# Optimization experiments

Measured on AMD Instinct MI355X. Metric: run time of the kernel, lower is better.

Reference implementation:

```python
import jax, jax.numpy as jnp
import numpy as np

B, T, D, MP = 32, 256, 512, 20


def setup_inputs() -> dict:
    key = jax.random.key(0)
    k1, k2, k3 = jax.random.split(key, 3)
    reps_lt = jax.random.normal(k1, (B, T, D), dtype=jnp.float32)
    reps_rt = jax.random.normal(k2, (B, T, D), dtype=jnp.float32)
    kernel = jax.random.normal(k3, (1, 1, 1, MP, D), dtype=jnp.float32)
    return {"reps_lt": reps_lt, "reps_rt": reps_rt, "kernel": kernel}


def reference(reps_lt, reps_rt, kernel):
    # kernel: (1,1,1,m,d) -> (m,d)
    km = kernel.reshape(kernel.shape[-2], kernel.shape[-1])
    # scores[b,t,s,m] = sum_d lt[b,t,d] * km[m,d] * rt[b,s,d]
    # matches original broadcast-multiply + sum over d (cosine_norm=False path)
    scores = jnp.einsum('btd,md,bsd->btsm', reps_lt, km, reps_rt)
    match = jnp.tanh(scores)               # [b, t1, t2, m]
    return jnp.max(match, axis=2)          # max-pool over t2 -> [b, t1, m]
```

## Files before the change

kernel.cpp:

```cpp
#include <hip/hip_runtime.h>


constexpr int TT = 256;
constexpr int DD = 512;
constexpr int NM = 20;
constexpr int NB = 32;
constexpr int BM = 64;

typedef float f32x4 __attribute__((ext_vector_type(4)));
typedef int   i32x8 __attribute__((ext_vector_type(8)));

__device__ __forceinline__ unsigned pack_bf16(float lo, float hi) {
    unsigned ulo = __builtin_bit_cast(unsigned, lo);
    unsigned uhi = __builtin_bit_cast(unsigned, hi);
    return (ulo >> 16) | (uhi & 0xFFFF0000u);
}

__device__ __forceinline__ unsigned pk4_fp8(float a, float b, float c, float d) {
    unsigned r = __builtin_amdgcn_cvt_pk_fp8_f32(a, b, 0, false);
    return __builtin_amdgcn_cvt_pk_fp8_f32(c, d, r, true);
}

__global__ __launch_bounds__(256)
void cast_rt(const float* __restrict__ rt, unsigned char* __restrict__ rtf)
{
    const int bid = (int)blockIdx.x;
    const int c8  = bid & 7;
    const int i   = bid >> 3;
    const int b   = c8 + 8 * (i & 3);
    const int sub = i >> 2;
    const int tid = threadIdx.x;
    const int lane = tid & 63;
    const int u6  = sub * 4 + (tid >> 6);
    const int s   = (u6 & 15) * 16 + (lane & 15);
    const int d0  = (u6 >> 4) * 128 + (lane >> 4) * 32;

    const float* p = rt + ((size_t)b * TT + s) * DD + d0;
    float4 x0 = *(const float4*)p;
    float4 x1 = *(const float4*)(p + 4);
    float4 x2 = *(const float4*)(p + 8);
    float4 x3 = *(const float4*)(p + 12);
    float4 x4 = *(const float4*)(p + 16);
    float4 x5 = *(const float4*)(p + 20);
    float4 x6 = *(const float4*)(p + 24);
    float4 x7 = *(const float4*)(p + 28);
    uint4 w0, w1;
    w0.x = pk4_fp8(x0.x, x0.y, x0.z, x0.w);
    w0.y = pk4_fp8(x1.x, x1.y, x1.z, x1.w);
    w0.z = pk4_fp8(x2.x, x2.y, x2.z, x2.w);
    w0.w = pk4_fp8(x3.x, x3.y, x3.z, x3.w);
    w1.x = pk4_fp8(x4.x, x4.y, x4.z, x4.w);
    w1.y = pk4_fp8(x5.x, x5.y, x5.z, x5.w);
    w1.z = pk4_fp8(x6.x, x6.y, x6.z, x6.w);
    w1.w = pk4_fp8(x7.x, x7.y, x7.z, x7.w);
    unsigned char* dst = rtf + ((size_t)b * 4096 + (size_t)u6 * 64 + lane) * 32;
    *(uint4*)dst        = w0;
    *(uint4*)(dst + 16) = w1;
}

__global__ __launch_bounds__(256, 3)
void mp_match_mx(const float* __restrict__ lt, const unsigned char* __restrict__ rtf,
                 const float* __restrict__ km, float* __restrict__ out)
{
    __shared__ __attribute__((aligned(32))) uint4 Ash[BM * 34];
    __shared__ __attribute__((aligned(16))) float maxbuf[4][BM];

    const int f  = blockIdx.x;
    const int c8 = f & 7;
    const int i  = f >> 3;
    const int b  = c8 + 8 * (i / 80);
    const int j  = i % 80;
    const int m  = j >> 2;
    const int t0 = (j & 3) * BM;

    const int tid  = threadIdx.x;
    const int w    = tid >> 6;
    const int lane = tid & 63;
    const int l15  = lane & 15;
    const int l4   = lane >> 4;

    const float* ltB = lt + ((size_t)b * TT + t0) * DD;
    const float* kmp = km + (size_t)m * DD;
    const unsigned char* rtB0 = rtf + (size_t)b * 131072 + (size_t)(w * 64 + lane) * 32;

    i32x8 ring[4];
    auto loadB = [&](int u) {
        ring[u & 3] = *(const i32x8*)(rtB0 + u * 8192);
    };

    loadB(0); loadB(1); loadB(2);

    const int cc = tid & 31, r0 = (tid >> 5) * 8;
    const float4 kA = *(const float4*)(kmp + cc * 16);
    const float4 kB = *(const float4*)(kmp + cc * 16 + 4);
    const float4 kC = *(const float4*)(kmp + cc * 16 + 8);
    const float4 kD = *(const float4*)(kmp + cc * 16 + 12);
#pragma unroll
    for (int r = 0; r < 8; ++r) {
        const float* src = ltB + (size_t)(r0 + r) * DD + cc * 16;
        float4 x0 = *(const float4*)src;
        float4 x1 = *(const float4*)(src + 4);
        float4 x2 = *(const float4*)(src + 8);
        float4 x3 = *(const float4*)(src + 12);
        uint4 o;
        o.x = pk4_fp8(x0.x * kA.x, x0.y * kA.y, x0.z * kA.z, x0.w * kA.w);
        o.y = pk4_fp8(x1.x * kB.x, x1.y * kB.y, x1.z * kB.z, x1.w * kB.w);
        o.z = pk4_fp8(x2.x * kC.x, x2.y * kC.y, x2.z * kC.z, x2.w * kC.w);
        o.w = pk4_fp8(x3.x * kD.x, x3.y * kD.y, x3.z * kD.z, x3.w * kD.w);
        Ash[(r0 + r) * 34 + cc] = o;
    }
    __syncthreads();

    f32x4 acc[4][4] = {};
    i32x8 av[4];

#pragma unroll
    for (int u = 0; u < 16; ++u) {
        const int kk = u >> 2, q = u & 3;
        if (u + 3 < 16) loadB(u + 3);
        if (q == 0) {
#pragma unroll
            for (int ii = 0; ii < 4; ++ii)
                av[ii] = *(const i32x8*)&Ash[(ii * 16 + l15) * 34 + kk * 8 + l4 * 2];
        }
        const i32x8 bv = ring[u & 3];
#pragma unroll
        for (int ii = 0; ii < 4; ++ii)
            acc[ii][q] = __builtin_amdgcn_mfma_scale_f32_16x16x128_f8f6f4(
                av[ii], bv, acc[ii][q], 0, 0, 0, 127, 0, 127);
    }

#pragma unroll
    for (int ii = 0; ii < 4; ++ii) {
        f32x4 v = acc[ii][0];
#pragma unroll
        for (int q = 1; q < 4; ++q) {
            v.x = fmaxf(v.x, acc[ii][q].x);
            v.y = fmaxf(v.y, acc[ii][q].y);
            v.z = fmaxf(v.z, acc[ii][q].z);
            v.w = fmaxf(v.w, acc[ii][q].w);
        }
#pragma unroll
        for (int off = 1; off < 16; off <<= 1) {
            v.x = fmaxf(v.x, __shfl_xor(v.x, off, 64));
            v.y = fmaxf(v.y, __shfl_xor(v.y, off, 64));
            v.z = fmaxf(v.z, __shfl_xor(v.z, off, 64));
            v.w = fmaxf(v.w, __shfl_xor(v.w, off, 64));
        }
        if (l15 == 0)
            *(f32x4*)&maxbuf[w][ii * 16 + l4 * 4] = v;
    }
    __syncthreads();
    if (tid < BM) {
        float v = fmaxf(fmaxf(maxbuf[0][tid], maxbuf[1][tid]),
                        fmaxf(maxbuf[2][tid], maxbuf[3][tid]));
        out[((size_t)b * TT + t0 + tid) * NM + m] = tanhf(v);
    }
}

typedef short bf16x8 __attribute__((ext_vector_type(8)));

__global__ __launch_bounds__(256, 2)
void mp_match_kernel(const float* __restrict__ lt, const float* __restrict__ rt,
                     const float* __restrict__ km, float* __restrict__ out)
{
    __shared__ __attribute__((aligned(16))) unsigned short Ash[2][4][128][8];
    __shared__ __attribute__((aligned(16))) unsigned short Bsh2[2][4][256][8];
    __shared__ __attribute__((aligned(16))) float maxbuf[2][128];

    const int ttile = blockIdx.x, m = blockIdx.y, b = blockIdx.z;
    const int t0 = ttile * 128;
    const int tid = threadIdx.x, wave = tid >> 6, lane = tid & 63;
    const int l15 = lane & 15, l4 = lane >> 4;
    const int wt = (wave & 1) * 64, wsi = wave >> 1;

    const float* ltp = lt + ((size_t)b * TT + t0) * DD;
    const float* rtp = rt + (size_t)b * TT * DD;
    const float* kmp = km + (size_t)m * DD;
    const int a_t = tid >> 1, a_h = tid & 1;

    f32x4 acc[4][8] = {};

    auto stage = [&](int kk, int buf) {
        const int d0 = kk * 32;
        const float* ap = ltp + (size_t)a_t * DD + d0 + a_h * 16;
        const float* kp = kmp + d0 + a_h * 16;
#pragma unroll
        for (int q = 0; q < 2; ++q) {
            float4 x0 = *(const float4*)(ap + q * 8);
            float4 x1 = *(const float4*)(ap + q * 8 + 4);
            float4 k0 = *(const float4*)(kp + q * 8);
            float4 k1 = *(const float4*)(kp + q * 8 + 4);
            uint4 wv;
            wv.x = pack_bf16(x0.x * k0.x, x0.y * k0.y);
            wv.y = pack_bf16(x0.z * k0.z, x0.w * k0.w);
            wv.z = pack_bf16(x1.x * k1.x, x1.y * k1.y);
            wv.w = pack_bf16(x1.z * k1.z, x1.w * k1.w);
            *(uint4*)&Ash[buf][a_h * 2 + q][a_t][0] = wv;
        }
        const float* bp = rtp + (size_t)tid * DD + d0;
#pragma unroll
        for (int p = 0; p < 4; ++p) {
            float4 y0 = *(const float4*)(bp + p * 8);
            float4 y1 = *(const float4*)(bp + p * 8 + 4);
            uint4 wv;
            wv.x = pack_bf16(y0.x, y0.y);
            wv.y = pack_bf16(y0.z, y0.w);
            wv.z = pack_bf16(y1.x, y1.y);
            wv.w = pack_bf16(y1.z, y1.w);
            *(uint4*)&Bsh2[buf][p][tid][0] = wv;
        }
    };

    stage(0, 0);
    for (int kk = 0; kk < 16; ++kk) {
        const int buf = kk & 1;
        __syncthreads();
        bf16x8 af[4], bfv[8];
#pragma unroll
        for (int i2 = 0; i2 < 4; ++i2)
            af[i2] = *(const bf16x8*)&Ash[buf][l4][wt + i2 * 16 + l15][0];
#pragma unroll
        for (int j2 = 0; j2 < 8; ++j2)
            bfv[j2] = *(const bf16x8*)&Bsh2[buf][l4][wsi * 128 + j2 * 16 + l15][0];
        if (kk + 1 < 16) stage(kk + 1, buf ^ 1);
#pragma unroll
        for (int i2 = 0; i2 < 4; ++i2)
#pragma unroll
            for (int j2 = 0; j2 < 8; ++j2)
                acc[i2][j2] = __builtin_amdgcn_mfma_f32_16x16x32_bf16(af[i2], bfv[j2], acc[i2][j2], 0, 0, 0);
    }
#pragma unroll
    for (int i2 = 0; i2 < 4; ++i2) {
        f32x4 v = acc[i2][0];
#pragma unroll
        for (int j2 = 1; j2 < 8; ++j2) {
            v.x = fmaxf(v.x, acc[i2][j2].x); v.y = fmaxf(v.y, acc[i2][j2].y);
            v.z = fmaxf(v.z, acc[i2][j2].z); v.w = fmaxf(v.w, acc[i2][j2].w);
        }
#pragma unroll
        for (int off = 1; off < 16; off <<= 1) {
            v.x = fmaxf(v.x, __shfl_xor(v.x, off, 64));
            v.y = fmaxf(v.y, __shfl_xor(v.y, off, 64));
            v.z = fmaxf(v.z, __shfl_xor(v.z, off, 64));
            v.w = fmaxf(v.w, __shfl_xor(v.w, off, 64));
        }
        if (l15 == 0) *(f32x4*)&maxbuf[wsi][wt + i2 * 16 + l4 * 4] = v;
    }
    __syncthreads();
    if (tid < 128) {
        float v = fmaxf(maxbuf[0][tid], maxbuf[1][tid]);
        out[((size_t)b * TT + t0 + tid) * NM + m] = tanhf(v);
    }
}

extern "C" void kernel_launch(void* const* d_in, const int* in_sizes, int n_in,
                              void* d_out, int out_size, void* d_ws, size_t ws_size,
                              hipStream_t stream) {
    const float* lt  = (const float*)d_in[0];
    const float* rt  = (const float*)d_in[1];
    const float* km  = (const float*)d_in[2];
    float*       out = (float*)d_out;

    const size_t elems = (size_t)NB * TT * DD;
    const size_t rtfB  = elems;

    if (ws_size >= rtfB) {
        unsigned char* rtf = (unsigned char*)d_ws;
        cast_rt<<<512, 256, 0, stream>>>(rt, rtf);
        mp_match_mx<<<2560, 256, 0, stream>>>(lt, rtf, km, out);
    } else {
        mp_match_kernel<<<dim3(2, NM, NB), 256, 0, stream>>>(lt, rt, km, out);
    }
}
```

Before: 113.8 us.

## Process five perspectives per block with double-buffered A tile and B register reuse

New measurement: 236.2 us. 2.08x slower.

```diff
diff --git a/kernel.cpp b/kernel.cpp
--- a/kernel.cpp
+++ b/kernel.cpp
@@ -6,6 +6,7 @@
 constexpr int NM = 20;
 constexpr int NB = 32;
 constexpr int BM = 64;
+constexpr int GM = 5;
 
 typedef float f32x4 __attribute__((ext_vector_type(4)));
 typedef int   i32x8 __attribute__((ext_vector_type(8)));
@@ -58,20 +59,20 @@
     *(uint4*)(dst + 16) = w1;
 }
 
-__global__ __launch_bounds__(256, 3)
+__global__ __launch_bounds__(256, 2)
 void mp_match_mx(const float* __restrict__ lt, const unsigned char* __restrict__ rtf,
                  const float* __restrict__ km, float* __restrict__ out)
 {
-    __shared__ __attribute__((aligned(32))) uint4 Ash[BM * 34];
-    __shared__ __attribute__((aligned(16))) float maxbuf[4][BM];
+    __shared__ __attribute__((aligned(32))) uint4 Ash[2][BM * 34];
+    __shared__ __attribute__((aligned(16))) float maxbuf[2][4][BM];
 
     const int f  = blockIdx.x;
     const int c8 = f & 7;
     const int i  = f >> 3;
-    const int b  = c8 + 8 * (i / 80);
-    const int j  = i % 80;
-    const int m  = j >> 2;
-    const int t0 = (j & 3) * BM;
+    const int b  = c8 + 8 * (i & 3);
+    const int r2 = i >> 2;
+    const int mg = r2 & 3;
+    const int t0 = (r2 >> 2) * BM;
 
     const int tid  = threadIdx.x;
     const int w    = tid >> 6;
@@ -80,7 +81,6 @@
     const int l4   = lane >> 4;
 
     const float* ltB = lt + ((size_t)b * TT + t0) * DD;
-    const float* kmp = km + (size_t)m * DD;
     const unsigned char* rtB0 = rtf + (size_t)b * 131072 + (size_t)(w * 64 + lane) * 32;
 
     i32x8 ring[4];
@@ -91,70 +91,115 @@
     loadB(0); loadB(1); loadB(2);
 
     const int cc = tid & 31, r0 = (tid >> 5) * 8;
-    const float4 kA = *(const float4*)(kmp + cc * 16);
-    const float4 kB = *(const float4*)(kmp + cc * 16 + 4);
-    const float4 kC = *(const float4*)(kmp + cc * 16 + 8);
-    const float4 kD = *(const float4*)(kmp + cc * 16 + 12);
-#pragma unroll
-    for (int r = 0; r < 8; ++r) {
-        const float* src = ltB + (size_t)(r0 + r) * DD + cc * 16;
-        float4 x0 = *(const float4*)src;
-        float4 x1 = *(const float4*)(src + 4);
-        float4 x2 = *(const float4*)(src + 8);
-        float4 x3 = *(const float4*)(src + 12);
-        uint4 o;
-        o.x = pk4_fp8(x0.x * kA.x, x0.y * kA.y, x0.z * kA.z, x0.w * kA.w);
-        o.y = pk4_fp8(x1.x * kB.x, x1.y * kB.y, x1.z * kB.z, x1.w * kB.w);
-        o.z = pk4_fp8(x2.x * kC.x, x2.y * kC.y, x2.z * kC.z, x2.w * kC.w);
-        o.w = pk4_fp8(x3.x * kD.x, x3.y * kD.y, x3.z * kD.z, x3.w * kD.w);
-        Ash[(r0 + r) * 34 + cc] = o;
+    {
+        const float* kmp = km + (size_t)(mg * GM) * DD + cc * 16;
+        const float4 kA = *(const float4*)(kmp);
+        const float4 kB = *(const float4*)(kmp + 4);
+        const float4 kC = *(const float4*)(kmp + 8);
+        const float4 kD = *(const float4*)(kmp + 12);
+#pragma unroll
+        for (int r = 0; r < 8; ++r) {
+            const float* src = ltB + (size_t)(r0 + r) * DD + cc * 16;
+            float4 x0 = *(const float4*)src;
+            float4 x1 = *(const float4*)(src + 4);
+            float4 x2 = *(const float4*)(src + 8);
+            float4 x3 = *(const float4*)(src + 12);
+            uint4 o;
+            o.x = pk4_fp8(x0.x * kA.x, x0.y * kA.y, x0.z * kA.z, x0.w * kA.w);
+            o.y = pk4_fp8(x1.x * kB.x, x1.y * kB.y, x1.z * kB.z, x1.w * kB.w);
+            o.z = pk4_fp8(x2.x * kC.x, x2.y * kC.y, x2.z * kC.z, x2.w * kC.w);
+            o.w = pk4_fp8(x3.x * kD.x, x3.y * kD.y, x3.z * kD.z, x3.w * kD.w);
+            Ash[0][(r0 + r) * 34 + cc] = o;
+        }
     }
     __syncthreads();
 
-    f32x4 acc[4][4] = {};
-    i32x8 av[4];
-
-#pragma unroll
-    for (int u = 0; u < 16; ++u) {
-        const int kk = u >> 2, q = u & 3;
-        if (u + 3 < 16) loadB(u + 3);
-        if (q == 0) {
+    for (int mi = 0; mi < GM; ++mi) {
+        const uint4* Acur = &Ash[mi & 1][0];
+        uint4*       Anx  = &Ash[(mi + 1) & 1][0];
+        const bool   more = (mi + 1 < GM);
+        const float* kmn  = km + (size_t)(mg * GM + mi + 1) * DD + cc * 16;
+
+        f32x4 acc[4][4] = {};
+        i32x8 av[4];
+        float4 kAn{}, kBn{}, kCn{}, kDn{};
+        float4 xr[2][4];
+
+#pragma unroll
+        for (int u = 0; u < 16; ++u) {
+            const int kk = u >> 2, q = u & 3;
+            const int un = u + 3;
+            if (un < 16) loadB(un);
+            else if (more) loadB(un - 16);
+
+            if (more) {
+                if (u == 0) {
+                    kAn = *(const float4*)(kmn);
+                    kBn = *(const float4*)(kmn + 4);
+                    kCn = *(const float4*)(kmn + 8);
+                    kDn = *(const float4*)(kmn + 12);
+                }
+                if (u >= 2 && u < 10) {
+                    const int r = u - 2;
+                    uint4 o;
+                    o.x = pk4_fp8(xr[r & 1][0].x * kAn.x, xr[r & 1][0].y * kAn.y,
+                                  xr[r & 1][0].z * kAn.z, xr[r & 1][0].w * kAn.w);
+                    o.y = pk4_fp8(xr[r & 1][1].x * kBn.x, xr[r & 1][1].y * kBn.y,
+                                  xr[r & 1][1].z * kBn.z, xr[r & 1][1].w * kBn.w);
+                    o.z = pk4_fp8(xr[r & 1][2].x * kCn.x, xr[r & 1][2].y * kCn.y,
+                                  xr[r & 1][2].z * kCn.z, xr[r & 1][2].w * kCn.w);
+                    o.w = pk4_fp8(xr[r & 1][3].x * kDn.x, xr[r & 1][3].y * kDn.y,
+                                  xr[r & 1][3].z * kDn.z, xr[r & 1][3].w * kDn.w);
+                    Anx[(r0 + r) * 34 + cc] = o;
+                }
+                if (u < 8) {
+                    const float* src = ltB + (size_t)(r0 + u) * DD + cc * 16;
+                    xr[u & 1][0] = *(const float4*)src;
+                    xr[u & 1][1] = *(const float4*)(src + 4);
+                    xr[u & 1][2] = *(const float4*)(src + 8);
+                    xr[u & 1][3] = *(const float4*)(src + 12);
+                }
+            }
+
+            if (q == 0) {
+#pragma unroll
+                for (int ii = 0; ii < 4; ++ii)
+                    av[ii] = *(const i32x8*)&Acur[(ii * 16 + l15) * 34 + kk * 8 + l4 * 2];
+            }
+            const i32x8 bv = ring[u & 3];
 #pragma unroll
             for (int ii = 0; ii < 4; ++ii)
-                av[ii] = *(const i32x8*)&Ash[(ii * 16 + l15) * 34 + kk * 8 + l4 * 2];
-        }
-        const i32x8 bv = ring[u & 3];
-#pragma unroll
-        for (int ii = 0; ii < 4; ++ii)
-            acc[ii][q] = __builtin_amdgcn_mfma_scale_f32_16x16x128_f8f6f4(
-                av[ii], bv, acc[ii][q], 0, 0, 0, 127, 0, 127);
-    }
-
-#pragma unroll
-    for (int ii = 0; ii < 4; ++ii) {
-        f32x4 v = acc[ii][0];
-#pragma unroll
-        for (int q = 1; q < 4; ++q) {
-            v.x = fmaxf(v.x, acc[ii][q].x);
-            v.y = fmaxf(v.y, acc[ii][q].y);
-            v.z = fmaxf(v.z, acc[ii][q].z);
-            v.w = fmaxf(v.w, acc[ii][q].w);
-        }
-#pragma unroll
-        for (int off = 1; off < 16; off <<= 1) {
-            v.x = fmaxf(v.x, __shfl_xor(v.x, off, 64));
-            v.y = fmaxf(v.y, __shfl_xor(v.y, off, 64));
-            v.z = fmaxf(v.z, __shfl_xor(v.z, off, 64));
-            v.w = fmaxf(v.w, __shfl_xor(v.w, off, 64));
-        }
-        if (l15 == 0)
-            *(f32x4*)&maxbuf[w][ii * 16 + l4 * 4] = v;
-    }
-    __syncthreads();
-    if (tid < BM) {
-        float v = fmaxf(fmaxf(maxbuf[0][tid], maxbuf[1][tid]),
-                        fmaxf(maxbuf[2][tid], maxbuf[3][tid]));
-        out[((size_t)b * TT + t0 + tid) * NM + m] = tanhf(v);
+                acc[ii][q] = __builtin_amdgcn_mfma_scale_f32_16x16x128_f8f6f4(
+                    av[ii], bv, acc[ii][q], 0, 0, 0, 127, 0, 127);
+        }
+
+        const int m = mg * GM + mi;
+#pragma unroll
+        for (int ii = 0; ii < 4; ++ii) {
+            f32x4 v = acc[ii][0];
+#pragma unroll
+            for (int q = 1; q < 4; ++q) {
+                v.x = fmaxf(v.x, acc[ii][q].x);
+                v.y = fmaxf(v.y, acc[ii][q].y);
+                v.z = fmaxf(v.z, acc[ii][q].z);
+                v.w = fmaxf(v.w, acc[ii][q].w);
+            }
+#pragma unroll
+            for (int off = 1; off < 16; off <<= 1) {
+                v.x = fmaxf(v.x, __shfl_xor(v.x, off, 64));
+                v.y = fmaxf(v.y, __shfl_xor(v.y, off, 64));
+                v.z = fmaxf(v.z, __shfl_xor(v.z, off, 64));
+                v.w = fmaxf(v.w, __shfl_xor(v.w, off, 64));
+            }
+            if (l15 == 0)
+                *(f32x4*)&maxbuf[mi & 1][w][ii * 16 + l4 * 4] = v;
+        }
+        __syncthreads();
+        if (tid < BM) {
+            float v = fmaxf(fmaxf(maxbuf[mi & 1][0][tid], maxbuf[mi & 1][1][tid]),
+                            fmaxf(maxbuf[mi & 1][2][tid], maxbuf[mi & 1][3][tid]));
+            out[((size_t)b * TT + t0 + tid) * NM + m] = tanhf(v);
+        }
     }
 }
 
@@ -268,7 +313,7 @@
     if (ws_size >= rtfB) {
         unsigned char* rtf = (unsigned char*)d_ws;
         cast_rt<<<512, 256, 0, stream>>>(rt, rtf);
-        mp_match_mx<<<2560, 256, 0, stream>>>(lt, rtf, km, out);
+        mp_match_mx<<<512, 256, 0, stream>>>(lt, rtf, km, out);
     } else {
         mp_match_kernel<<<dim3(2, NM, NB), 256, 0, stream>>>(lt, rt, km, out);
     }
```

## Process five projection rows per block with double-buffered fp8 A staging

Applied to the files above, without the earlier changes.

After: 304.7 us. 2.68x slower.

```diff
diff --git a/kernel.cpp b/kernel.cpp
--- a/kernel.cpp
+++ b/kernel.cpp
@@ -6,9 +6,13 @@
 constexpr int NM = 20;
 constexpr int NB = 32;
 constexpr int BM = 64;
+constexpr int GM = 5;
 
 typedef float f32x4 __attribute__((ext_vector_type(4)));
 typedef int   i32x8 __attribute__((ext_vector_type(8)));
+
+struct TrueT  { static constexpr bool value = true;  };
+struct FalseT { static constexpr bool value = false; };
 
 __device__ __forceinline__ unsigned pack_bf16(float lo, float hi) {
     unsigned ulo = __builtin_bit_cast(unsigned, lo);
@@ -58,20 +62,20 @@
     *(uint4*)(dst + 16) = w1;
 }
 
-__global__ __launch_bounds__(256, 3)
+__global__ __launch_bounds__(256, 2)
 void mp_match_mx(const float* __restrict__ lt, const unsigned char* __restrict__ rtf,
                  const float* __restrict__ km, float* __restrict__ out)
 {
-    __shared__ __attribute__((aligned(32))) uint4 Ash[BM * 34];
-    __shared__ __attribute__((aligned(16))) float maxbuf[4][BM];
+    __shared__ __attribute__((aligned(32))) uint4 Ash[2][BM * 34];
+    __shared__ __attribute__((aligned(16))) float maxbuf[2][4][BM];
 
     const int f  = blockIdx.x;
     const int c8 = f & 7;
     const int i  = f >> 3;
-    const int b  = c8 + 8 * (i / 80);
-    const int j  = i % 80;
-    const int m  = j >> 2;
-    const int t0 = (j & 3) * BM;
+    const int b  = c8 + 8 * (i & 3);
+    const int r2 = i >> 2;
+    const int mg = r2 & 3;
+    const int t0 = (r2 >> 2) * BM;
 
     const int tid  = threadIdx.x;
     const int w    = tid >> 6;
@@ -80,7 +84,6 @@
     const int l4   = lane >> 4;
 
     const float* ltB = lt + ((size_t)b * TT + t0) * DD;
-    const float* kmp = km + (size_t)m * DD;
     const unsigned char* rtB0 = rtf + (size_t)b * 131072 + (size_t)(w * 64 + lane) * 32;
 
     i32x8 ring[4];
@@ -91,71 +94,93 @@
     loadB(0); loadB(1); loadB(2);
 
     const int cc = tid & 31, r0 = (tid >> 5) * 8;
-    const float4 kA = *(const float4*)(kmp + cc * 16);
-    const float4 kB = *(const float4*)(kmp + cc * 16 + 4);
-    const float4 kC = *(const float4*)(kmp + cc * 16 + 8);
-    const float4 kD = *(const float4*)(kmp + cc * 16 + 12);
-#pragma unroll
-    for (int r = 0; r < 8; ++r) {
+    auto stageRow = [&](int r, const float* kmRow, uint4* dstA) {
+        const float* kp  = kmRow + cc * 16;
         const float* src = ltB + (size_t)(r0 + r) * DD + cc * 16;
+        float4 k0 = *(const float4*)(kp);
+        float4 k1 = *(const float4*)(kp + 4);
+        float4 k2 = *(const float4*)(kp + 8);
+        float4 k3 = *(const float4*)(kp + 12);
         float4 x0 = *(const float4*)src;
         float4 x1 = *(const float4*)(src + 4);
         float4 x2 = *(const float4*)(src + 8);
         float4 x3 = *(const float4*)(src + 12);
         uint4 o;
-        o.x = pk4_fp8(x0.x * kA.x, x0.y * kA.y, x0.z * kA.z, x0.w * kA.w);
-        o.y = pk4_fp8(x1.x * kB.x, x1.y * kB.y, x1.z * kB.z, x1.w * kB.w);
-        o.z = pk4_fp8(x2.x * kC.x, x2.y * kC.y, x2.z * kC.z, x2.w * kC.w);
-        o.w = pk4_fp8(x3.x * kD.x, x3.y * kD.y, x3.z * kD.z, x3.w * kD.w);
-        Ash[(r0 + r) * 34 + cc] = o;
+        o.x = pk4_fp8(x0.x * k0.x, x0.y * k0.y, x0.z * k0.z, x0.w * k0.w);
+        o.y = pk4_fp8(x1.x * k1.x, x1.y * k1.y, x1.z * k1.z, x1.w * k1.w);
+        o.z = pk4_fp8(x2.x * k2.x, x2.y * k2.y, x2.z * k2.z, x2.w * k2.w);
+        o.w = pk4_fp8(x3.x * k3.x, x3.y * k3.y, x3.z * k3.z, x3.w * k3.w);
+        dstA[(r0 + r) * 34 + cc] = o;
+    };
+
+    {
+        const float* km0 = km + (size_t)(mg * GM) * DD;
+#pragma unroll
+        for (int r = 0; r < 8; ++r) stageRow(r, km0, &Ash[0][0]);
     }
     __syncthreads();
 
-    f32x4 acc[4][4] = {};
-    i32x8 av[4];
-
-#pragma unroll
-    for (int u = 0; u < 16; ++u) {
-        const int kk = u >> 2, q = u & 3;
-        if (u + 3 < 16) loadB(u + 3);
-        if (q == 0) {
+    auto phase = [&](int mi, auto STAGE) {
+        constexpr bool stg = decltype(STAGE)::value;
+        const uint4* Acur = &Ash[mi & 1][0];
+        uint4*       Anx  = &Ash[(mi + 1) & 1][0];
+        const float* kmn  = km + (size_t)(mg * GM + mi + 1) * DD;
+
+        f32x4 acc[4][4] = {};
+        i32x8 av[4];
+
+#pragma unroll
+        for (int u = 0; u < 16; ++u) {
+            const int kk = u >> 2, q = u & 3;
+            const int un = u + 3;
+            if (un < 16) loadB(un);
+            else loadB(un - 16);
+
+            if (stg && u < 8) stageRow(u, kmn, Anx);
+
+            if (q == 0) {
+#pragma unroll
+                for (int ii = 0; ii < 4; ++ii)
+                    av[ii] = *(const i32x8*)&Acur[(ii * 16 + l15) * 34 + kk * 8 + l4 * 2];
+            }
+            const i32x8 bv = ring[u & 3];
 #pragma unroll
             for (int ii = 0; ii < 4; ++ii)
-                av[ii] = *(const i32x8*)&Ash[(ii * 16 + l15) * 34 + kk * 8 + l4 * 2];
-        }
-        const i32x8 bv = ring[u & 3];
-#pragma unroll
-        for (int ii = 0; ii < 4; ++ii)
-            acc[ii][q] = __builtin_amdgcn_mfma_scale_f32_16x16x128_f8f6f4(
-                av[ii], bv, acc[ii][q], 0, 0, 0, 127, 0, 127);
-    }
-
-#pragma unroll
-    for (int ii = 0; ii < 4; ++ii) {
-        f32x4 v = acc[ii][0];
-#pragma unroll
-        for (int q = 1; q < 4; ++q) {
-            v.x = fmaxf(v.x, acc[ii][q].x);
-            v.y = fmaxf(v.y, acc[ii][q].y);
-            v.z = fmaxf(v.z, acc[ii][q].z);
-            v.w = fmaxf(v.w, acc[ii][q].w);
-        }
-#pragma unroll
-        for (int off = 1; off < 16; off <<= 1) {
-            v.x = fmaxf(v.x, __shfl_xor(v.x, off, 64));
-            v.y = fmaxf(v.y, __shfl_xor(v.y, off, 64));
-            v.z = fmaxf(v.z, __shfl_xor(v.z, off, 64));
-            v.w = fmaxf(v.w, __shfl_xor(v.w, off, 64));
-        }
-        if (l15 == 0)
-            *(f32x4*)&maxbuf[w][ii * 16 + l4 * 4] = v;
-    }
-    __syncthreads();
-    if (tid < BM) {
-        float v = fmaxf(fmaxf(maxbuf[0][tid], maxbuf[1][tid]),
-                        fmaxf(maxbuf[2][tid], maxbuf[3][tid]));
-        out[((size_t)b * TT + t0 + tid) * NM + m] = tanhf(v);
-    }
+                acc[ii][q] = __builtin_amdgcn_mfma_scale_f32_16x16x128_f8f6f4(
+                    av[ii], bv, acc[ii][q], 0, 0, 0, 127, 0, 127);
+        }
+
+        const int m = mg * GM + mi;
+#pragma unroll
+        for (int ii = 0; ii < 4; ++ii) {
+            f32x4 v = acc[ii][0];
+#pragma unroll
+            for (int q = 1; q < 4; ++q) {
+                v.x = fmaxf(v.x, acc[ii][q].x);
+                v.y = fmaxf(v.y, acc[ii][q].y);
+                v.z = fmaxf(v.z, acc[ii][q].z);
+                v.w = fmaxf(v.w, acc[ii][q].w);
+            }
+#pragma unroll
+            for (int off = 1; off < 16; off <<= 1) {
+                v.x = fmaxf(v.x, __shfl_xor(v.x, off, 64));
+                v.y = fmaxf(v.y, __shfl_xor(v.y, off, 64));
+                v.z = fmaxf(v.z, __shfl_xor(v.z, off, 64));
+                v.w = fmaxf(v.w, __shfl_xor(v.w, off, 64));
+            }
+            if (l15 == 0)
+                *(f32x4*)&maxbuf[mi & 1][w][ii * 16 + l4 * 4] = v;
+        }
+        __syncthreads();
+        if (tid < BM) {
+            float v = fmaxf(fmaxf(maxbuf[mi & 1][0][tid], maxbuf[mi & 1][1][tid]),
+                            fmaxf(maxbuf[mi & 1][2][tid], maxbuf[mi & 1][3][tid]));
+            out[((size_t)b * TT + t0 + tid) * NM + m] = tanhf(v);
+        }
+    };
+
+    for (int mi = 0; mi < GM - 1; ++mi) phase(mi, TrueT{});
+    phase(GM - 1, FalseT{});
 }
 
 typedef short bf16x8 __attribute__((ext_vector_type(8)));
@@ -268,7 +293,7 @@
     if (ws_size >= rtfB) {
         unsigned char* rtf = (unsigned char*)d_ws;
         cast_rt<<<512, 256, 0, stream>>>(rt, rtf);
-        mp_match_mx<<<2560, 256, 0, stream>>>(lt, rtf, km, out);
+        mp_match_mx<<<512, 256, 0, stream>>>(lt, rtf, km, out);
     } else {
         mp_match_kernel<<<dim3(2, NM, NB), 256, 0, stream>>>(lt, rt, km, out);
     }
```

## Pre-cast lt to bf16 in a fused cast kernel, use DPP row max and setprio

Applied to the files above, without the earlier changes.

Measured after the change: 108.5 us. -4.6%, faster.

```diff
diff --git a/kernel.cpp b/kernel.cpp
--- a/kernel.cpp
+++ b/kernel.cpp
@@ -6,6 +6,7 @@
 constexpr int NM = 20;
 constexpr int NB = 32;
 constexpr int BM = 64;
+constexpr int NK = 4;
 
 typedef float f32x4 __attribute__((ext_vector_type(4)));
 typedef int   i32x8 __attribute__((ext_vector_type(8)));
@@ -15,51 +16,80 @@
     unsigned uhi = __builtin_bit_cast(unsigned, hi);
     return (ulo >> 16) | (uhi & 0xFFFF0000u);
 }
+__device__ __forceinline__ float blo(unsigned u) { return __builtin_bit_cast(float, u << 16); }
+__device__ __forceinline__ float bhi(unsigned u) { return __builtin_bit_cast(float, u); }
 
 __device__ __forceinline__ unsigned pk4_fp8(float a, float b, float c, float d) {
     unsigned r = __builtin_amdgcn_cvt_pk_fp8_f32(a, b, 0, false);
     return __builtin_amdgcn_cvt_pk_fp8_f32(c, d, r, true);
 }
 
+__device__ __forceinline__ float row_max16(float v) {
+    int t;
+    t = __builtin_amdgcn_update_dpp(0, __builtin_bit_cast(int, v), 0x121, 0xf, 0xf, true);
+    v = fmaxf(v, __builtin_bit_cast(float, t));
+    t = __builtin_amdgcn_update_dpp(0, __builtin_bit_cast(int, v), 0x122, 0xf, 0xf, true);
+    v = fmaxf(v, __builtin_bit_cast(float, t));
+    t = __builtin_amdgcn_update_dpp(0, __builtin_bit_cast(int, v), 0x124, 0xf, 0xf, true);
+    v = fmaxf(v, __builtin_bit_cast(float, t));
+    t = __builtin_amdgcn_update_dpp(0, __builtin_bit_cast(int, v), 0x128, 0xf, 0xf, true);
+    v = fmaxf(v, __builtin_bit_cast(float, t));
+    return v;
+}
+
 __global__ __launch_bounds__(256)
-void cast_rt(const float* __restrict__ rt, unsigned char* __restrict__ rtf)
+void cast_inputs(const float* __restrict__ lt, const float* __restrict__ rt,
+                 unsigned short* __restrict__ ltb, unsigned char* __restrict__ rtf)
 {
     const int bid = (int)blockIdx.x;
-    const int c8  = bid & 7;
-    const int i   = bid >> 3;
-    const int b   = c8 + 8 * (i & 3);
-    const int sub = i >> 2;
     const int tid = threadIdx.x;
-    const int lane = tid & 63;
-    const int u6  = sub * 4 + (tid >> 6);
-    const int s   = (u6 & 15) * 16 + (lane & 15);
-    const int d0  = (u6 >> 4) * 128 + (lane >> 4) * 32;
-
-    const float* p = rt + ((size_t)b * TT + s) * DD + d0;
-    float4 x0 = *(const float4*)p;
-    float4 x1 = *(const float4*)(p + 4);
-    float4 x2 = *(const float4*)(p + 8);
-    float4 x3 = *(const float4*)(p + 12);
-    float4 x4 = *(const float4*)(p + 16);
-    float4 x5 = *(const float4*)(p + 20);
-    float4 x6 = *(const float4*)(p + 24);
-    float4 x7 = *(const float4*)(p + 28);
-    uint4 w0, w1;
-    w0.x = pk4_fp8(x0.x, x0.y, x0.z, x0.w);
-    w0.y = pk4_fp8(x1.x, x1.y, x1.z, x1.w);
-    w0.z = pk4_fp8(x2.x, x2.y, x2.z, x2.w);
-    w0.w = pk4_fp8(x3.x, x3.y, x3.z, x3.w);
-    w1.x = pk4_fp8(x4.x, x4.y, x4.z, x4.w);
-    w1.y = pk4_fp8(x5.x, x5.y, x5.z, x5.w);
-    w1.z = pk4_fp8(x6.x, x6.y, x6.z, x6.w);
-    w1.w = pk4_fp8(x7.x, x7.y, x7.z, x7.w);
-    unsigned char* dst = rtf + ((size_t)b * 4096 + (size_t)u6 * 64 + lane) * 32;
-    *(uint4*)dst        = w0;
-    *(uint4*)(dst + 16) = w1;
-}
-
-__global__ __launch_bounds__(256, 3)
-void mp_match_mx(const float* __restrict__ lt, const unsigned char* __restrict__ rtf,
+    if (bid < 2048) {
+        size_t base = ((size_t)bid * 256 + tid) * 8;
+        float4 a = *(const float4*)(lt + base);
+        float4 b = *(const float4*)(lt + base + 4);
+        uint4 w;
+        w.x = pack_bf16(a.x, a.y);
+        w.y = pack_bf16(a.z, a.w);
+        w.z = pack_bf16(b.x, b.y);
+        w.w = pack_bf16(b.z, b.w);
+        *(uint4*)(ltb + base) = w;
+    } else {
+        const int bid2 = bid - 2048;
+        const int c8   = bid2 & 7;
+        const int i    = bid2 >> 3;
+        const int b    = c8 + 8 * (i & 3);
+        const int sub  = i >> 2;
+        const int lane = tid & 63;
+        const int u6   = sub * 4 + (tid >> 6);
+        const int s    = (u6 & 15) * 16 + (lane & 15);
+        const int d0   = (u6 >> 4) * 128 + (lane >> 4) * 32;
+
+        const float* p = rt + ((size_t)b * TT + s) * DD + d0;
+        float4 x0 = *(const float4*)p;
+        float4 x1 = *(const float4*)(p + 4);
+        float4 x2 = *(const float4*)(p + 8);
+        float4 x3 = *(const float4*)(p + 12);
+        float4 x4 = *(const float4*)(p + 16);
+        float4 x5 = *(const float4*)(p + 20);
+        float4 x6 = *(const float4*)(p + 24);
+        float4 x7 = *(const float4*)(p + 28);
+        uint4 w0, w1;
+        w0.x = pk4_fp8(x0.x, x0.y, x0.z, x0.w);
+        w0.y = pk4_fp8(x1.x, x1.y, x1.z, x1.w);
+        w0.z = pk4_fp8(x2.x, x2.y, x2.z, x2.w);
+        w0.w = pk4_fp8(x3.x, x3.y, x3.z, x3.w);
+        w1.x = pk4_fp8(x4.x, x4.y, x4.z, x4.w);
+        w1.y = pk4_fp8(x5.x, x5.y, x5.z, x5.w);
+        w1.z = pk4_fp8(x6.x, x6.y, x6.z, x6.w);
+        w1.w = pk4_fp8(x7.x, x7.y, x7.z, x7.w);
+        unsigned char* dst = rtf + ((size_t)b * 4096 + (size_t)u6 * 64 + lane) * 32;
+        *(uint4*)dst        = w0;
+        *(uint4*)(dst + 16) = w1;
+    }
+}
+
+__global__ __launch_bounds__(256, 2)
+void mp_match_mx(const unsigned short* __restrict__ ltb, const unsigned char* __restrict__ rtf,
                  const float* __restrict__ km, float* __restrict__ out)
 {
     __shared__ __attribute__((aligned(32))) uint4 Ash[BM * 34];
@@ -79,9 +109,9 @@
     const int l15  = lane & 15;
     const int l4   = lane >> 4;
 
-    const float* ltB = lt + ((size_t)b * TT + t0) * DD;
-    const float* kmp = km + (size_t)m * DD;
-    const unsigned char* rtB0 = rtf + (size_t)b * 131072 + (size_t)(w * 64 + lane) * 32;
+    const unsigned short* ltB = ltb + ((size_t)b * TT + t0) * DD;
+    const float*          kmp = km  + (size_t)m * DD;
+    const unsigned char*  rtB0 = rtf + (size_t)b * 131072 + (size_t)(w * 64 + lane) * 32;
 
     i32x8 ring[4];
     auto loadB = [&](int u) {
@@ -97,16 +127,14 @@
     const float4 kD = *(const float4*)(kmp + cc * 16 + 12);
 #pragma unroll
     for (int r = 0; r < 8; ++r) {
-        const float* src = ltB + (size_t)(r0 + r) * DD + cc * 16;
-        float4 x0 = *(const float4*)src;
-        float4 x1 = *(const float4*)(src + 4);
-        float4 x2 = *(const float4*)(src + 8);
-        float4 x3 = *(const float4*)(src + 12);
+        const unsigned short* src = ltB + (size_t)(r0 + r) * DD + cc * 16;
+        uint4 h0 = *(const uint4*)src;
+        uint4 h1 = *(const uint4*)(src + 8);
         uint4 o;
-        o.x = pk4_fp8(x0.x * kA.x, x0.y * kA.y, x0.z * kA.z, x0.w * kA.w);
-        o.y = pk4_fp8(x1.x * kB.x, x1.y * kB.y, x1.z * kB.z, x1.w * kB.w);
-        o.z = pk4_fp8(x2.x * kC.x, x2.y * kC.y, x2.z * kC.z, x2.w * kC.w);
-        o.w = pk4_fp8(x3.x * kD.x, x3.y * kD.y, x3.z * kD.z, x3.w * kD.w);
+        o.x = pk4_fp8(blo(h0.x) * kA.x, bhi(h0.x) * kA.y, blo(h0.y) * kA.z, bhi(h0.y) * kA.w);
+        o.y = pk4_fp8(blo(h0.z) * kB.x, bhi(h0.z) * kB.y, blo(h0.w) * kB.z, bhi(h0.w) * kB.w);
+        o.z = pk4_fp8(blo(h1.x) * kC.x, bhi(h1.x) * kC.y, blo(h1.y) * kC.z, bhi(h1.y) * kC.w);
+        o.w = pk4_fp8(blo(h1.z) * kD.x, bhi(h1.z) * kD.y, blo(h1.w) * kD.z, bhi(h1.w) * kD.w);
         Ash[(r0 + r) * 34 + cc] = o;
     }
     __syncthreads();
@@ -124,10 +152,12 @@
                 av[ii] = *(const i32x8*)&Ash[(ii * 16 + l15) * 34 + kk * 8 + l4 * 2];
         }
         const i32x8 bv = ring[u & 3];
+        __builtin_amdgcn_s_setprio(1);
 #pragma unroll
         for (int ii = 0; ii < 4; ++ii)
             acc[ii][q] = __builtin_amdgcn_mfma_scale_f32_16x16x128_f8f6f4(
                 av[ii], bv, acc[ii][q], 0, 0, 0, 127, 0, 127);
+        __builtin_amdgcn_s_setprio(0);
     }
 
 #pragma unroll
@@ -140,13 +170,10 @@
             v.z = fmaxf(v.z, acc[ii][q].z);
             v.w = fmaxf(v.w, acc[ii][q].w);
         }
-#pragma unroll
-        for (int off = 1; off < 16; off <<= 1) {
-            v.x = fmaxf(v.x, __shfl_xor(v.x, off, 64));
-            v.y = fmaxf(v.y, __shfl_xor(v.y, off, 64));
-            v.z = fmaxf(v.z, __shfl_xor(v.z, off, 64));
-            v.w = fmaxf(v.w, __shfl_xor(v.w, off, 64));
-        }
+        v.x = row_max16(v.x);
+        v.y = row_max16(v.y);
+        v.z = row_max16(v.z);
+        v.w = row_max16(v.w);
         if (l15 == 0)
             *(f32x4*)&maxbuf[w][ii * 16 + l4 * 4] = v;
     }
@@ -263,12 +290,14 @@
     float*       out = (float*)d_out;
 
     const size_t elems = (size_t)NB * TT * DD;
+    const size_t ltbB  = elems * sizeof(unsigned short);
     const size_t rtfB  = elems;
 
-    if (ws_size >= rtfB) {
-        unsigned char* rtf = (unsigned char*)d_ws;
-        cast_rt<<<512, 256, 0, stream>>>(rt, rtf);
-        mp_match_mx<<<2560, 256, 0, stream>>>(lt, rtf, km, out);
+    if (ws_size >= ltbB + rtfB) {
+        unsigned short* ltb = (unsigned short*)d_ws;
+        unsigned char*  rtf = (unsigned char*)((char*)d_ws + ltbB);
+        cast_inputs<<<2560, 256, 0, stream>>>(lt, rt, ltb, rtf);
+        mp_match_mx<<<2560, 256, 0, stream>>>(ltb, rtf, km, out);
     } else {
         mp_match_kernel<<<dim3(2, NM, NB), 256, 0, stream>>>(lt, rt, km, out);
     }
```
